# Kernel tuning notes

Measured on AMD Instinct MI355X. Metric: run time of the kernel, lower is better.

## Reference

```python
import jax, jax.numpy as jnp
import numpy as np

S, B, D, N, DH = 1024, 2, 1024, 16, 64  # seq, batch, d_model, n_head, d_head
EPS = 1e-5


def setup_inputs() -> dict:
    key = jax.random.key(0)
    k0, k1, k2, k3 = jax.random.split(key, 4)
    h = jax.random.normal(k0, (S, B, D), dtype=jnp.float32)
    Wq = jax.random.normal(k1, (N * DH, D), dtype=jnp.float32) * 0.02
    Wkv = jax.random.normal(k2, (2 * N * DH, D), dtype=jnp.float32) * 0.02
    Wo = jax.random.normal(k3, (D, N * DH), dtype=jnp.float32) * 0.02
    gamma = jnp.ones((D,), dtype=jnp.float32)
    beta = jnp.zeros((D,), dtype=jnp.float32)
    return {"h": h, "Wq": Wq, "Wkv": Wkv, "Wo": Wo, "gamma": gamma, "beta": beta}


def reference(h, Wq, Wkv, Wo, gamma, beta):
    scale = 1.0 / np.sqrt(DH).astype(np.float32)
    # projections (torch Linear: x @ W.T), no mems so c == h
    q = (h @ Wq.T).reshape(S, B, N, DH)
    kv = h @ Wkv.T                      # [S,B,2*N*DH]
    k, v = jnp.split(kv, 2, axis=-1)
    k = k.reshape(S, B, N, DH)
    v = v.reshape(S, B, N, DH)
    # full attention scores [i,j,b,n]
    score = jnp.einsum('ibnd,jbnd->ijbn', q, k) * scale
    prob = jax.nn.softmax(score, axis=1)  # softmax over keys j
    # twicing correction (layer_num >= 14): P <- 2P - P @ P per (b,n)
    p = prob.transpose(2, 3, 0, 1)       # [b,n,i,j]
    p = 2.0 * p - jnp.matmul(p, p)
    prob = p.transpose(2, 3, 0, 1)       # back to [i,j,b,n]
    # attention output
    vec = jnp.einsum('ijbn,jbnd->ibnd', prob, v).reshape(S, B, N * DH)
    attn_out = vec @ Wo.T                # [S,B,D]
    # post-LN residual
    x = h + attn_out
    mu = jnp.mean(x, axis=-1, keepdims=True)
    var = jnp.mean(jnp.square(x - mu), axis=-1, keepdims=True)
    return (x - mu) / jnp.sqrt(var + EPS) * gamma + beta
```

## Files before the change

kernel.cpp:

```cpp
#include <hip/hip_runtime.h>

typedef unsigned short u16;
typedef unsigned int u32;
typedef __attribute__((ext_vector_type(8))) short short8;
typedef __attribute__((ext_vector_type(4))) float f32x4;

constexpr int kS = 1024, kB = 2, kN = 16, kDH = 64, kD = 1024;
constexpr float kEps = 1e-5f;

__device__ __forceinline__ u16 f2b(float f) {
  u32 u = __float_as_uint(f);
  u += 0x7fffu + ((u >> 16) & 1u);
  return (u16)(u >> 16);
}
__device__ __forceinline__ float b2f(u32 bits) {
  return __uint_as_float(bits << 16);
}

__device__ __forceinline__ void gload16(const u16* g, u16* l) {
  __builtin_amdgcn_global_load_lds(
      (const __attribute__((address_space(1))) void*)g,
      (__attribute__((address_space(3))) void*)l, 16, 0, 0);
}

__device__ __forceinline__ short8 read8sw(const u16* base, int row, int colel) {
  return *(const short8*)(base + (row << 6) + (colel ^ ((row & 7) << 3)));
}

__global__ __launch_bounds__(256) void cvt_all(const float* __restrict__ h,
                                               const float* __restrict__ wq,
                                               const float* __restrict__ wkv,
                                               const float* __restrict__ wo,
                                               u16* __restrict__ hb, u16* __restrict__ wqb,
                                               u16* __restrict__ wkvb, u16* __restrict__ wob) {
  long idx = (long)blockIdx.x * 256 + threadIdx.x;
  const float* in;
  u16* out;
  long base;
  if (idx < 524288L) { in = h; out = hb; base = idx; }
  else if (idx < 786432L) { in = wq; out = wqb; base = idx - 524288L; }
  else if (idx < 1310720L) { in = wkv; out = wkvb; base = idx - 786432L; }
  else { in = wo; out = wob; base = idx - 1310720L; }
  float4 v = *(const float4*)(in + base * 4);
  uint2 o;
  o.x = (u32)f2b(v.x) | ((u32)f2b(v.y) << 16);
  o.y = (u32)f2b(v.z) | ((u32)f2b(v.w) << 16);
  *(uint2*)(out + base * 4) = o;
}

struct GemmParams {
  const u16* A; long ldA;
  const u16* B; long ldB;
  int K;
  u16* ob; float* of; long ldO;
  u16* aux_b16;
};

template <int MODE, int BM, int BN, int WC, int MF, int NF>
__global__ __launch_bounds__(256) void gemm_tile(GemmParams p) {
  __shared__ __align__(16) u16 sm[2][(BM + BN) * 32];
  const u16* A = p.A;
  const u16* B = p.B;
  const int tid = threadIdx.x;
  const int lane = tid & 63;
  const int w = tid >> 6;
  const int wR = w / WC, wC = w % WC;
  const int lr = lane & 15, lk = lane >> 4;
  const int bm0 = blockIdx.y * BM, bn0 = blockIdx.x * BN;
  const int m0 = bm0 + wR * (MF * 16), n0 = bn0 + wC * (NF * 16);

  f32x4 acc[MF][NF];
#pragma unroll
  for (int i = 0; i < MF; ++i)
#pragma unroll
    for (int j = 0; j < NF; ++j) acc[i][j] = (f32x4){0.f, 0.f, 0.f, 0.f};

  constexpr int ACH = BM * 4;
  constexpr int NCH = (BM + BN) * 4;
  constexpr int NLD = NCH / 256;

  auto stage = [&](int k0, int buf) {
#pragma unroll
    for (int i = 0; i < NLD; ++i) {
      const int cbase = i * 256 + w * 64;
      const int c = cbase + lane;
      const u16* g;
      if (cbase < ACH) {
        g = A + (long)(bm0 + (c >> 2)) * p.ldA + k0 + (c & 3) * 8;
      } else {
        const int cc = c - ACH;
        g = B + (long)(bn0 + (cc >> 2)) * p.ldB + k0 + (cc & 3) * 8;
      }
      gload16(g, &sm[buf][cbase * 8]);
    }
  };

  auto compute = [&](int buf) {
    const u16* As = sm[buf];
    const u16* Bs = sm[buf] + BM * 32;
    short8 af[MF], bf[NF];
#pragma unroll
    for (int mi = 0; mi < MF; ++mi)
      af[mi] = *(const short8*)(As + ((wR * MF + mi) * 16 + lr) * 32 + lk * 8);
#pragma unroll
    for (int ni = 0; ni < NF; ++ni)
      bf[ni] = *(const short8*)(Bs + ((wC * NF + ni) * 16 + lr) * 32 + lk * 8);
#pragma unroll
    for (int mi = 0; mi < MF; ++mi)
#pragma unroll
      for (int ni = 0; ni < NF; ++ni)
        acc[mi][ni] = __builtin_amdgcn_mfma_f32_16x16x32_bf16(af[mi], bf[ni], acc[mi][ni], 0, 0, 0);
  };

  const int nt = p.K / 32;
  stage(0, 0);
  __syncthreads();
  for (int t = 0; t < nt - 1; ++t) {
    stage((t + 1) * 32, (t & 1) ^ 1);
    compute(t & 1);
    __syncthreads();
  }
  compute((nt - 1) & 1);

#pragma unroll
  for (int mi = 0; mi < MF; ++mi)
#pragma unroll
    for (int ni = 0; ni < NF; ++ni)
#pragma unroll
      for (int r = 0; r < 4; ++r) {
        int row = m0 + mi * 16 + lk * 4 + r;
        int col = n0 + ni * 16 + lr;
        float v = acc[mi][ni][r];
        if constexpr (MODE == 0) {
          p.ob[(long)row * p.ldO + col] = f2b(v);
        } else if constexpr (MODE == 1) {
          if (col < kD) {
            p.ob[(long)row * kD + col] = f2b(v);
          } else {
            int c = col - kD, n = c >> 6, dd = c & 63, s = row >> 1, b = row & 1;
            p.aux_b16[(((long)((b * kN + n) * kDH + dd)) << 10) + s] = f2b(v);
          }
        } else {
          p.of[(long)row * p.ldO + col] = v;
        }
      }
}

template <bool SECOND>
__global__ __launch_bounds__(256) void flash_tw(const u16* __restrict__ qp,
                                                const u16* __restrict__ kp,
                                                const u16* __restrict__ bp,
                                                float* __restrict__ linv_g,
                                                u16* __restrict__ outp) {
  __shared__ __align__(16) u16 Qs[32 * 64];
  __shared__ __align__(16) u16 Ks[2][64 * 64];
  __shared__ __align__(16) u16 Bs[2][64 * 64];
  __shared__ __align__(16) u16 Ss[32 * 64];
  const int z = blockIdx.y;
  const int qb0 = blockIdx.x * 32;
  const int tid = threadIdx.x, lane = tid & 63, w = tid >> 6;
  const int lr = lane & 15, lk = lane >> 4;
  const int wR = w >> 1, wC = w & 1;

  {
    int c = w * 64 + lane;
    int row = c >> 3, col = (c & 7) ^ (row & 7);
    gload16(qp + (long)(qb0 + row) * 2048 + z * 64 + col * 8, Qs + c * 8);
  }
  auto stageKB = [&](int j, int buf) {
#pragma unroll
    for (int i = 0; i < 2; ++i) {
      int c = i * 256 + w * 64 + lane;
      int row = c >> 3, col = (c & 7) ^ (row & 7);
      gload16(kp + (long)(j * 64 + row) * 2048 + z * 64 + col * 8, Ks[buf] + c * 8);
      gload16(bp + (long)z * 65536 + (long)row * 1024 + j * 64 + col * 8, Bs[buf] + c * 8);
    }
  };
  stageKB(0, 0);
  __syncthreads();

  f32x4 acc[2];
  acc[0] = (f32x4){0.f, 0.f, 0.f, 0.f};
  acc[1] = (f32x4){0.f, 0.f, 0.f, 0.f};
  float lsum = 0.f;
  const int q = wC * 16 + lr;

  for (int j = 0; j < 16; ++j) {
    const int cur = j & 1;
    if (j < 15) stageKB(j + 1, cur ^ 1);
    f32x4 st[2];
    st[0] = (f32x4){0.f, 0.f, 0.f, 0.f};
    st[1] = (f32x4){0.f, 0.f, 0.f, 0.f};
#pragma unroll
    for (int kk = 0; kk < 2; ++kk) {
      short8 qf = read8sw(Qs, q, kk * 32 + lk * 8);
#pragma unroll
      for (int ki = 0; ki < 2; ++ki) {
        short8 kf = read8sw(Ks[cur], wR * 32 + ki * 16 + lr, kk * 32 + lk * 8);
        st[ki] = __builtin_amdgcn_mfma_f32_16x16x32_bf16(kf, qf, st[ki], 0, 0, 0);
      }
    }
#pragma unroll
    for (int ki = 0; ki < 2; ++ki) {
      float e0 = __expf(st[ki][0] * 0.125f);
      float e1 = __expf(st[ki][1] * 0.125f);
      float e2 = __expf(st[ki][2] * 0.125f);
      float e3 = __expf(st[ki][3] * 0.125f);
      if (!SECOND) lsum += e0 + e1 + e2 + e3;
      int k0 = wR * 32 + ki * 16 + lk * 4;
      uint2 pk;
      pk.x = (u32)f2b(e0) | ((u32)f2b(e1) << 16);
      pk.y = (u32)f2b(e2) | ((u32)f2b(e3) << 16);
      *(uint2*)(Ss + ((q << 6) + (k0 ^ ((q & 7) << 3)))) = pk;
    }
    __syncthreads();
#pragma unroll
    for (int kk = 0; kk < 2; ++kk) {
      short8 sf = read8sw(Ss, wR * 16 + lr, kk * 32 + lk * 8);
#pragma unroll
      for (int ni = 0; ni < 2; ++ni) {
        short8 bf = read8sw(Bs[cur], wC * 32 + ni * 16 + lr, kk * 32 + lk * 8);
        acc[ni] = __builtin_amdgcn_mfma_f32_16x16x32_bf16(sf, bf, acc[ni], 0, 0, 0);
      }
    }
    __syncthreads();
  }

  float* lred = (float*)Ss;
  if (!SECOND) {
    lsum += __shfl_xor(lsum, 16);
    lsum += __shfl_xor(lsum, 32);
    if (lane < 16) lred[wR * 32 + wC * 16 + lr] = lsum;
    __syncthreads();
    if (tid < 32) {
      float inv = 1.f / (lred[tid] + lred[32 + tid]);
      lred[64 + tid] = inv;
      linv_g[(long)z * 1024 + qb0 + tid] = inv;
    }
    __syncthreads();
  }

  const int q0 = wR * 16 + lk * 4;
#pragma unroll
  for (int ni = 0; ni < 2; ++ni) {
    const int d = wC * 32 + ni * 16 + lr;
    if (!SECOND) {
      const float* linv_s = lred + 64;
      u32 lo = (u32)f2b(acc[ni][0] * linv_s[q0]) | ((u32)f2b(acc[ni][1] * linv_s[q0 + 1]) << 16);
      u32 hi = (u32)f2b(acc[ni][2] * linv_s[q0 + 2]) | ((u32)f2b(acc[ni][3] * linv_s[q0 + 3]) << 16);
      uint2 pk; pk.x = lo; pk.y = hi;
      *(uint2*)(outp + (long)z * 65536 + (long)d * 1024 + qb0 + q0) = pk;
    } else {
      float4 l4 = *(const float4*)(linv_g + (long)z * 1024 + qb0 + q0);
      uint2 ut = *(const uint2*)(bp + (long)z * 65536 + (long)d * 1024 + qb0 + q0);
      float u0 = b2f(ut.x & 0xffffu), u1 = b2f(ut.x >> 16);
      float u2 = b2f(ut.y & 0xffffu), u3 = b2f(ut.y >> 16);
      long ob = (long)(qb0 + q0) * 2048 + z * 64 + d;
      outp[ob]        = f2b(2.f * u0 - acc[ni][0] * l4.x);
      outp[ob + 2048] = f2b(2.f * u1 - acc[ni][1] * l4.y);
      outp[ob + 4096] = f2b(2.f * u2 - acc[ni][2] * l4.z);
      outp[ob + 6144] = f2b(2.f * u3 - acc[ni][3] * l4.w);
    }
  }
}

__global__ __launch_bounds__(256) void resid_ln(const float* __restrict__ h,
                                                const float* __restrict__ attn,
                                                const float* __restrict__ gamma,
                                                const float* __restrict__ beta,
                                                float* __restrict__ out) {
  __shared__ float rs[4], rs2[4];
  const long row = blockIdx.x;
  const int t = threadIdx.x;
  long base = (row << 10) + t * 4;
  float4 hv = *(const float4*)(h + base);
  float4 av = *(const float4*)(attn + base);
  float x0 = hv.x + av.x, x1 = hv.y + av.y, x2 = hv.z + av.z, x3 = hv.w + av.w;
  float s = x0 + x1 + x2 + x3;
  float s2 = x0 * x0 + x1 * x1 + x2 * x2 + x3 * x3;
  for (int o = 32; o; o >>= 1) { s += __shfl_xor(s, o); s2 += __shfl_xor(s2, o); }
  int wid = t >> 6;
  if ((t & 63) == 0) { rs[wid] = s; rs2[wid] = s2; }
  __syncthreads();
  s = rs[0] + rs[1] + rs[2] + rs[3];
  s2 = rs2[0] + rs2[1] + rs2[2] + rs2[3];
  float mean = s * (1.f / 1024.f);
  float var = s2 * (1.f / 1024.f) - mean * mean;
  float rstd = rsqrtf(var + kEps);
  int d = t * 4;
  float4 g = *(const float4*)(gamma + d);
  float4 bt = *(const float4*)(beta + d);
  float4 o_;
  o_.x = (x0 - mean) * rstd * g.x + bt.x;
  o_.y = (x1 - mean) * rstd * g.y + bt.y;
  o_.z = (x2 - mean) * rstd * g.z + bt.z;
  o_.w = (x3 - mean) * rstd * g.w + bt.w;
  *(float4*)(out + base) = o_;
}

extern "C" void kernel_launch(void* const* d_in, const int* in_sizes, int n_in,
                              void* d_out, int out_size, void* d_ws, size_t ws_size,
                              hipStream_t stream) {
  const float* h = (const float*)d_in[0];
  const float* Wq = (const float*)d_in[1];
  const float* Wkv = (const float*)d_in[2];
  const float* Wo = (const float*)d_in[3];
  const float* gamma = (const float*)d_in[4];
  const float* beta = (const float*)d_in[5];
  float* out = (float*)d_out;

  char* ws = (char*)d_ws;
  size_t off = 0;
  auto alloc = [&](size_t bytes) -> void* {
    void* p = ws + off;
    off = (off + bytes + 255) & ~(size_t)255;
    return p;
  };
  u16* hb = (u16*)alloc(2097152ULL * 2);
  u16* Wqb = (u16*)alloc(1048576ULL * 2);
  u16* Wkvb = (u16*)alloc(2097152ULL * 2);
  u16* Wob = (u16*)alloc(1048576ULL * 2);
  u16* qb = (u16*)alloc(2097152ULL * 2);
  u16* kb = (u16*)alloc(2097152ULL * 2);
  u16* vtb = (u16*)alloc(2097152ULL * 2);
  u16* Ut = (u16*)alloc(2097152ULL * 2);
  float* linv = (float*)alloc(32768ULL * 4);
  u16* vecb = (u16*)alloc(2097152ULL * 2);
  float* attn = (float*)alloc(2097152ULL * 4);
  (void)ws_size; (void)n_in; (void)in_sizes; (void)out_size;

  cvt_all<<<6144, 256, 0, stream>>>(h, Wq, Wkv, Wo, hb, Wqb, Wkvb, Wob);

  {
    GemmParams p{};
    p.A = hb; p.ldA = 1024;
    p.B = Wqb; p.ldB = 1024;
    p.K = 1024; p.ob = qb; p.ldO = 1024;
    gemm_tile<0, 64, 64, 2, 2, 2><<<dim3(16, 32, 1), 256, 0, stream>>>(p);
  }
  {
    GemmParams p{};
    p.A = hb; p.ldA = 1024;
    p.B = Wkvb; p.ldB = 1024;
    p.K = 1024; p.ob = kb; p.aux_b16 = vtb;
    gemm_tile<1, 64, 64, 2, 2, 2><<<dim3(32, 32, 1), 256, 0, stream>>>(p);
  }
  flash_tw<false><<<dim3(32, 32), 256, 0, stream>>>(qb, kb, vtb, linv, Ut);
  flash_tw<true><<<dim3(32, 32), 256, 0, stream>>>(qb, kb, Ut, linv, vecb);
  {
    GemmParams p{};
    p.A = vecb; p.ldA = 1024;
    p.B = Wob; p.ldB = 1024;
    p.K = 1024; p.of = attn; p.ldO = 1024;
    gemm_tile<5, 64, 64, 2, 2, 2><<<dim3(16, 32, 1), 256, 0, stream>>>(p);
  }
  resid_ln<<<2048, 256, 0, stream>>>(h, attn, gamma, beta, out);
}
```

Before: 112.2 us.

## Fuse Q and KV projections into one GEMM and double flash query tile

Merges the separate Q and KV projection GEMMs into a single launch (mode 6) that picks the weight pointer per column block and routes outputs to q, k and transposed v. The flash twicing kernel now processes 64 queries per block instead of 32, with Q fragments held in registers and a 2x2 MFMA accumulator per wave. K and B tiles are reused across twice as many queries. The cost is half as many blocks (512) and more registers and LDS per block, which may lower occupancy.

```diff
diff --git a/kernel.cpp b/kernel.cpp
--- a/kernel.cpp
+++ b/kernel.cpp
@@ -5,7 +5,7 @@
 typedef __attribute__((ext_vector_type(8))) short short8;
 typedef __attribute__((ext_vector_type(4))) float f32x4;
 
-constexpr int kS = 1024, kB = 2, kN = 16, kDH = 64, kD = 1024;
+constexpr int kN = 16, kDH = 64, kD = 1024;
 constexpr float kEps = 1e-5f;
 
 __device__ __forceinline__ u16 f2b(float f) {
@@ -51,8 +51,10 @@
 struct GemmParams {
   const u16* A; long ldA;
   const u16* B; long ldB;
+  const u16* B2;
   int K;
   u16* ob; float* of; long ldO;
+  u16* ob2;
   u16* aux_b16;
 };
 
@@ -60,7 +62,6 @@
 __global__ __launch_bounds__(256) void gemm_tile(GemmParams p) {
   __shared__ __align__(16) u16 sm[2][(BM + BN) * 32];
   const u16* A = p.A;
-  const u16* B = p.B;
   const int tid = threadIdx.x;
   const int lane = tid & 63;
   const int w = tid >> 6;
@@ -68,6 +69,7 @@
   const int lr = lane & 15, lk = lane >> 4;
   const int bm0 = blockIdx.y * BM, bn0 = blockIdx.x * BN;
   const int m0 = bm0 + wR * (MF * 16), n0 = bn0 + wC * (NF * 16);
+  const u16* B = (MODE == 6 && bn0 >= 1024) ? (p.B2 - 1048576) : p.B;
 
   f32x4 acc[MF][NF];
 #pragma unroll
@@ -131,13 +133,13 @@
         int row = m0 + mi * 16 + lk * 4 + r;
         int col = n0 + ni * 16 + lr;
         float v = acc[mi][ni][r];
-        if constexpr (MODE == 0) {
-          p.ob[(long)row * p.ldO + col] = f2b(v);
-        } else if constexpr (MODE == 1) {
-          if (col < kD) {
-            p.ob[(long)row * kD + col] = f2b(v);
+        if constexpr (MODE == 6) {
+          if (col < 1024) {
+            p.ob[(long)row * 1024 + col] = f2b(v);
+          } else if (col < 2048) {
+            p.ob2[(long)row * 1024 + (col - 1024)] = f2b(v);
           } else {
-            int c = col - kD, n = c >> 6, dd = c & 63, s = row >> 1, b = row & 1;
+            int c = col - 2048, n = c >> 6, dd = c & 63, s = row >> 1, b = row & 1;
             p.aux_b16[(((long)((b * kN + n) * kDH + dd)) << 10) + s] = f2b(v);
           }
         } else {
@@ -152,18 +154,19 @@
                                                 const u16* __restrict__ bp,
                                                 float* __restrict__ linv_g,
                                                 u16* __restrict__ outp) {
-  __shared__ __align__(16) u16 Qs[32 * 64];
+  __shared__ __align__(16) u16 Qs[64 * 64];
   __shared__ __align__(16) u16 Ks[2][64 * 64];
   __shared__ __align__(16) u16 Bs[2][64 * 64];
-  __shared__ __align__(16) u16 Ss[32 * 64];
+  __shared__ __align__(16) u16 Ss[64 * 64];
   const int z = blockIdx.y;
-  const int qb0 = blockIdx.x * 32;
+  const int qb0 = blockIdx.x * 64;
   const int tid = threadIdx.x, lane = tid & 63, w = tid >> 6;
   const int lr = lane & 15, lk = lane >> 4;
   const int wR = w >> 1, wC = w & 1;
 
-  {
-    int c = w * 64 + lane;
+#pragma unroll
+  for (int i = 0; i < 2; ++i) {
+    int c = i * 256 + w * 64 + lane;
     int row = c >> 3, col = (c & 7) ^ (row & 7);
     gload16(qp + (long)(qb0 + row) * 2048 + z * 64 + col * 8, Qs + c * 8);
   }
@@ -179,87 +182,108 @@
   stageKB(0, 0);
   __syncthreads();
 
-  f32x4 acc[2];
-  acc[0] = (f32x4){0.f, 0.f, 0.f, 0.f};
-  acc[1] = (f32x4){0.f, 0.f, 0.f, 0.f};
-  float lsum = 0.f;
-  const int q = wC * 16 + lr;
+  short8 qf[2][2];
+#pragma unroll
+  for (int qi = 0; qi < 2; ++qi)
+#pragma unroll
+    for (int kk = 0; kk < 2; ++kk)
+      qf[qi][kk] = read8sw(Qs, wC * 32 + qi * 16 + lr, kk * 32 + lk * 8);
+
+  f32x4 acc[2][2];
+#pragma unroll
+  for (int i = 0; i < 2; ++i)
+#pragma unroll
+    for (int j = 0; j < 2; ++j) acc[i][j] = (f32x4){0.f, 0.f, 0.f, 0.f};
+  float lsum[2] = {0.f, 0.f};
 
   for (int j = 0; j < 16; ++j) {
     const int cur = j & 1;
     if (j < 15) stageKB(j + 1, cur ^ 1);
-    f32x4 st[2];
-    st[0] = (f32x4){0.f, 0.f, 0.f, 0.f};
-    st[1] = (f32x4){0.f, 0.f, 0.f, 0.f};
-#pragma unroll
-    for (int kk = 0; kk < 2; ++kk) {
-      short8 qf = read8sw(Qs, q, kk * 32 + lk * 8);
+    f32x4 st[2][2];
+#pragma unroll
+    for (int a = 0; a < 2; ++a)
+#pragma unroll
+      for (int b = 0; b < 2; ++b) st[a][b] = (f32x4){0.f, 0.f, 0.f, 0.f};
+#pragma unroll
+    for (int kk = 0; kk < 2; ++kk)
 #pragma unroll
       for (int ki = 0; ki < 2; ++ki) {
         short8 kf = read8sw(Ks[cur], wR * 32 + ki * 16 + lr, kk * 32 + lk * 8);
-        st[ki] = __builtin_amdgcn_mfma_f32_16x16x32_bf16(kf, qf, st[ki], 0, 0, 0);
-      }
-    }
-#pragma unroll
-    for (int ki = 0; ki < 2; ++ki) {
-      float e0 = __expf(st[ki][0] * 0.125f);
-      float e1 = __expf(st[ki][1] * 0.125f);
-      float e2 = __expf(st[ki][2] * 0.125f);
-      float e3 = __expf(st[ki][3] * 0.125f);
-      if (!SECOND) lsum += e0 + e1 + e2 + e3;
-      int k0 = wR * 32 + ki * 16 + lk * 4;
-      uint2 pk;
-      pk.x = (u32)f2b(e0) | ((u32)f2b(e1) << 16);
-      pk.y = (u32)f2b(e2) | ((u32)f2b(e3) << 16);
-      *(uint2*)(Ss + ((q << 6) + (k0 ^ ((q & 7) << 3)))) = pk;
-    }
+#pragma unroll
+        for (int qi = 0; qi < 2; ++qi)
+          st[ki][qi] = __builtin_amdgcn_mfma_f32_16x16x32_bf16(kf, qf[qi][kk], st[ki][qi], 0, 0, 0);
+      }
+#pragma unroll
+    for (int ki = 0; ki < 2; ++ki)
+#pragma unroll
+      for (int qi = 0; qi < 2; ++qi) {
+        float e0 = __expf(st[ki][qi][0] * 0.125f);
+        float e1 = __expf(st[ki][qi][1] * 0.125f);
+        float e2 = __expf(st[ki][qi][2] * 0.125f);
+        float e3 = __expf(st[ki][qi][3] * 0.125f);
+        if (!SECOND) lsum[qi] += e0 + e1 + e2 + e3;
+        int q = wC * 32 + qi * 16 + lr;
+        int k0 = wR * 32 + ki * 16 + lk * 4;
+        uint2 pk;
+        pk.x = (u32)f2b(e0) | ((u32)f2b(e1) << 16);
+        pk.y = (u32)f2b(e2) | ((u32)f2b(e3) << 16);
+        *(uint2*)(Ss + ((q << 6) + (k0 ^ ((q & 7) << 3)))) = pk;
+      }
     __syncthreads();
 #pragma unroll
     for (int kk = 0; kk < 2; ++kk) {
-      short8 sf = read8sw(Ss, wR * 16 + lr, kk * 32 + lk * 8);
-#pragma unroll
-      for (int ni = 0; ni < 2; ++ni) {
-        short8 bf = read8sw(Bs[cur], wC * 32 + ni * 16 + lr, kk * 32 + lk * 8);
-        acc[ni] = __builtin_amdgcn_mfma_f32_16x16x32_bf16(sf, bf, acc[ni], 0, 0, 0);
-      }
+      short8 sf0 = read8sw(Ss, wR * 32 + lr, kk * 32 + lk * 8);
+      short8 sf1 = read8sw(Ss, wR * 32 + 16 + lr, kk * 32 + lk * 8);
+      short8 bf0 = read8sw(Bs[cur], wC * 32 + lr, kk * 32 + lk * 8);
+      short8 bf1 = read8sw(Bs[cur], wC * 32 + 16 + lr, kk * 32 + lk * 8);
+      acc[0][0] = __builtin_amdgcn_mfma_f32_16x16x32_bf16(sf0, bf0, acc[0][0], 0, 0, 0);
+      acc[0][1] = __builtin_amdgcn_mfma_f32_16x16x32_bf16(sf0, bf1, acc[0][1], 0, 0, 0);
+      acc[1][0] = __builtin_amdgcn_mfma_f32_16x16x32_bf16(sf1, bf0, acc[1][0], 0, 0, 0);
+      acc[1][1] = __builtin_amdgcn_mfma_f32_16x16x32_bf16(sf1, bf1, acc[1][1], 0, 0, 0);
     }
     __syncthreads();
   }
 
   float* lred = (float*)Ss;
   if (!SECOND) {
-    lsum += __shfl_xor(lsum, 16);
-    lsum += __shfl_xor(lsum, 32);
-    if (lane < 16) lred[wR * 32 + wC * 16 + lr] = lsum;
-    __syncthreads();
-    if (tid < 32) {
-      float inv = 1.f / (lred[tid] + lred[32 + tid]);
-      lred[64 + tid] = inv;
+#pragma unroll
+    for (int qi = 0; qi < 2; ++qi) {
+      lsum[qi] += __shfl_xor(lsum[qi], 16);
+      lsum[qi] += __shfl_xor(lsum[qi], 32);
+      if (lane < 16) lred[wR * 64 + wC * 32 + qi * 16 + lr] = lsum[qi];
+    }
+    __syncthreads();
+    if (tid < 64) {
+      float inv = 1.f / (lred[tid] + lred[64 + tid]);
+      lred[128 + tid] = inv;
       linv_g[(long)z * 1024 + qb0 + tid] = inv;
     }
     __syncthreads();
   }
 
-  const int q0 = wR * 16 + lk * 4;
-#pragma unroll
-  for (int ni = 0; ni < 2; ++ni) {
-    const int d = wC * 32 + ni * 16 + lr;
-    if (!SECOND) {
-      const float* linv_s = lred + 64;
-      u32 lo = (u32)f2b(acc[ni][0] * linv_s[q0]) | ((u32)f2b(acc[ni][1] * linv_s[q0 + 1]) << 16);
-      u32 hi = (u32)f2b(acc[ni][2] * linv_s[q0 + 2]) | ((u32)f2b(acc[ni][3] * linv_s[q0 + 3]) << 16);
-      uint2 pk; pk.x = lo; pk.y = hi;
-      *(uint2*)(outp + (long)z * 65536 + (long)d * 1024 + qb0 + q0) = pk;
-    } else {
-      float4 l4 = *(const float4*)(linv_g + (long)z * 1024 + qb0 + q0);
-      uint2 ut = *(const uint2*)(bp + (long)z * 65536 + (long)d * 1024 + qb0 + q0);
-      float u0 = b2f(ut.x & 0xffffu), u1 = b2f(ut.x >> 16);
-      float u2 = b2f(ut.y & 0xffffu), u3 = b2f(ut.y >> 16);
-      long ob = (long)(qb0 + q0) * 2048 + z * 64 + d;
-      outp[ob]        = f2b(2.f * u0 - acc[ni][0] * l4.x);
-      outp[ob + 2048] = f2b(2.f * u1 - acc[ni][1] * l4.y);
-      outp[ob + 4096] = f2b(2.f * u2 - acc[ni][2] * l4.z);
-      outp[ob + 6144] = f2b(2.f * u3 - acc[ni][3] * l4.w);
+#pragma unroll
+  for (int qi = 0; qi < 2; ++qi) {
+    const int q0 = wR * 32 + qi * 16 + lk * 4;
+#pragma unroll
+    for (int ni = 0; ni < 2; ++ni) {
+      const int d = wC * 32 + ni * 16 + lr;
+      if (!SECOND) {
+        const float* linv_s = lred + 128;
+        u32 lo = (u32)f2b(acc[qi][ni][0] * linv_s[q0]) | ((u32)f2b(acc[qi][ni][1] * linv_s[q0 + 1]) << 16);
+        u32 hi = (u32)f2b(acc[qi][ni][2] * linv_s[q0 + 2]) | ((u32)f2b(acc[qi][ni][3] * linv_s[q0 + 3]) << 16);
+        uint2 pk; pk.x = lo; pk.y = hi;
+        *(uint2*)(outp + (long)z * 65536 + (long)d * 1024 + qb0 + q0) = pk;
+      } else {
+        float4 l4 = *(const float4*)(linv_g + (long)z * 1024 + qb0 + q0);
+        uint2 ut = *(const uint2*)(bp + (long)z * 65536 + (long)d * 1024 + qb0 + q0);
+        float u0 = b2f(ut.x & 0xffffu), u1 = b2f(ut.x >> 16);
+        float u2 = b2f(ut.y & 0xffffu), u3 = b2f(ut.y >> 16);
+        long ob = (long)(qb0 + q0) * 2048 + z * 64 + d;
+        outp[ob]        = f2b(2.f * u0 - acc[qi][ni][0] * l4.x);
+        outp[ob + 2048] = f2b(2.f * u1 - acc[qi][ni][1] * l4.y);
+        outp[ob + 4096] = f2b(2.f * u2 - acc[qi][ni][2] * l4.z);
+        outp[ob + 6144] = f2b(2.f * u3 - acc[qi][ni][3] * l4.w);
+      }
     }
   }
 }
@@ -334,19 +358,12 @@
   {
     GemmParams p{};
     p.A = hb; p.ldA = 1024;
-    p.B = Wqb; p.ldB = 1024;
-    p.K = 1024; p.ob = qb; p.ldO = 1024;
-    gemm_tile<0, 64, 64, 2, 2, 2><<<dim3(16, 32, 1), 256, 0, stream>>>(p);
-  }
-  {
-    GemmParams p{};
-    p.A = hb; p.ldA = 1024;
-    p.B = Wkvb; p.ldB = 1024;
-    p.K = 1024; p.ob = kb; p.aux_b16 = vtb;
-    gemm_tile<1, 64, 64, 2, 2, 2><<<dim3(32, 32, 1), 256, 0, stream>>>(p);
-  }
-  flash_tw<false><<<dim3(32, 32), 256, 0, stream>>>(qb, kb, vtb, linv, Ut);
-  flash_tw<true><<<dim3(32, 32), 256, 0, stream>>>(qb, kb, Ut, linv, vecb);
+    p.B = Wqb; p.ldB = 1024; p.B2 = Wkvb;
+    p.K = 1024; p.ob = qb; p.ob2 = kb; p.aux_b16 = vtb;
+    gemm_tile<6, 64, 64, 2, 2, 2><<<dim3(48, 32, 1), 256, 0, stream>>>(p);
+  }
+  flash_tw<false><<<dim3(16, 32), 256, 0, stream>>>(qb, kb, vtb, linv, Ut);
+  flash_tw<true><<<dim3(16, 32), 256, 0, stream>>>(qb, kb, Ut, linv, vecb);
   {
     GemmParams p{};
     p.A = vecb; p.ldA = 1024;
```

New measurement: 110.4 us. No clear change (-1.6%).
